# Performance work log

Measured on AMD Instinct MI355X. Metric: run time of the kernel, lower is better.

The kernel has to match this reference:

```python
import jax, jax.numpy as jnp
import numpy as np

N_NODES = 50000
N_EDGES = 800000
IN_NODE = 256
IN_EDGE = 64
OUT_DIM = 128


def setup_inputs() -> dict:
    key = jax.random.key(0)
    k1, k2, k3, k4, k5, k6, k7 = jax.random.split(key, 7)
    feats_node = jax.random.normal(k1, (N_NODES, IN_NODE), dtype=jnp.float32)
    feats_edge = jax.random.normal(k2, (N_EDGES, IN_EDGE), dtype=jnp.float32)
    src = jax.random.randint(k3, (N_EDGES,), 0, N_NODES, dtype=jnp.int32)
    dst = jax.random.randint(k4, (N_EDGES,), 0, N_NODES, dtype=jnp.int32)
    # weights init: normal(std=0.5), torch Linear stores [out, in]
    Wn = 0.5 * jax.random.normal(k5, (OUT_DIM, IN_NODE), dtype=jnp.float32)
    We = 0.5 * jax.random.normal(k6, (IN_EDGE, IN_EDGE), dtype=jnp.float32)
    Wa = 0.5 * jax.random.normal(k7, (1, 2 * OUT_DIM + IN_EDGE), dtype=jnp.float32)
    return {"feats_node": feats_node, "feats_edge": feats_edge,
            "src": src, "dst": dst, "Wn": Wn, "We": We, "Wa": Wa}


def reference(feats_node, feats_edge, src, dst, Wn, We, Wa):
    n_nodes = feats_node.shape[0]
    # node / edge projections
    z = feats_node @ Wn.T            # [N, out_dim]
    ze = feats_edge @ We.T           # [E, in_dim_edge]
    # per-edge attention logit: attn_fc(cat(z_src, z_dst, z_edge)) + leaky_relu
    z3 = jnp.concatenate([z[src], z[dst], ze], axis=1)   # [E, 2*out+edge]
    a = z3 @ Wa.T                                        # [E, 1]
    e = jax.nn.leaky_relu(a, negative_slope=0.2)[:, 0]   # [E]
    # segment softmax over incoming edges of each dst node (numerically stable)
    m = jax.ops.segment_max(e, dst, num_segments=n_nodes)        # [N]
    m = jnp.where(jnp.isfinite(m), m, 0.0)                       # isolated nodes
    e_exp = jnp.exp(e - m[dst])                                  # [E]
    denom = jax.ops.segment_sum(e_exp, dst, num_segments=n_nodes)  # [N]
    alpha = e_exp / jnp.maximum(denom[dst], 1e-38)               # [E]
    # weighted scatter-sum of source messages
    h = jax.ops.segment_sum(alpha[:, None] * z[src], dst, num_segments=n_nodes)
    return h, ze
```

## Files before the change

### kernel.cpp

```cpp
#include <hip/hip_runtime.h>
#include <hip/hip_bf16.h>
#include <math.h>

#define N_NODES 50000
#define N_EDGES 800000
#define IN_NODE 256
#define IN_EDGE 64
#define OUT_DIM 128

#define K1_MT 64
#define K1_KT 32

__global__ __launch_bounds__(256) void k1_node_gemm(
    const float* __restrict__ fn, const float* __restrict__ Wn,
    const float* __restrict__ Wa,
    __hip_bfloat16* __restrict__ zb,
    float* __restrict__ s_src, float* __restrict__ s_dst)
{
    __shared__ float A_s[K1_KT][K1_MT + 4];
    __shared__ float B_s[K1_KT][OUT_DIM + 4];
    __shared__ float red_s[K1_MT][17];
    __shared__ float red_d[K1_MT][17];

    const int t  = threadIdx.x;
    const int m0 = blockIdx.x * K1_MT;
    const int tn = t & 15;
    const int tm = t >> 4;
    const int r0 = tm * 4;
    const int c0 = tn * 8;

    float acc[4][8];
    for (int i = 0; i < 4; ++i)
        for (int j = 0; j < 8; ++j) acc[i][j] = 0.f;

    for (int k0 = 0; k0 < IN_NODE; k0 += K1_KT) {
        {
            const int chunk = t & 7;
            const int nd    = t >> 3;
            for (int hh = 0; hh < 2; ++hh) {
                const int node = nd + hh * 32;
                int gr = m0 + node; if (gr >= N_NODES) gr = N_NODES - 1;
                const float4 v = *(const float4*)&fn[(size_t)gr * IN_NODE + k0 + chunk * 4];
                A_s[chunk * 4 + 0][node] = v.x;
                A_s[chunk * 4 + 1][node] = v.y;
                A_s[chunk * 4 + 2][node] = v.z;
                A_s[chunk * 4 + 3][node] = v.w;
            }
        }
        {
            const int chunk = t & 7;
            const int cb    = t >> 3;
            for (int hh = 0; hh < 4; ++hh) {
                const int c = cb + hh * 32;
                const float4 v = *(const float4*)&Wn[(size_t)c * IN_NODE + k0 + chunk * 4];
                B_s[chunk * 4 + 0][c] = v.x;
                B_s[chunk * 4 + 1][c] = v.y;
                B_s[chunk * 4 + 2][c] = v.z;
                B_s[chunk * 4 + 3][c] = v.w;
            }
        }
        __syncthreads();

        for (int k = 0; k < K1_KT; ++k) {
            const float4 a  = *(const float4*)&A_s[k][r0];
            const float4 b0 = *(const float4*)&B_s[k][c0];
            const float4 b1 = *(const float4*)&B_s[k][c0 + 4];
            const float av[4] = {a.x, a.y, a.z, a.w};
            const float bv[8] = {b0.x, b0.y, b0.z, b0.w, b1.x, b1.y, b1.z, b1.w};
            for (int i = 0; i < 4; ++i)
                for (int j = 0; j < 8; ++j)
                    acc[i][j] += av[i] * bv[j];
        }
        __syncthreads();
    }

    float wa_s[8], wa_d[8];
    for (int j = 0; j < 8; ++j) {
        wa_s[j] = Wa[c0 + j];
        wa_d[j] = Wa[OUT_DIM + c0 + j];
    }
    float ps[4], pd[4];
    for (int i = 0; i < 4; ++i) {
        float a = 0.f, b = 0.f;
        for (int j = 0; j < 8; ++j) {
            a += wa_s[j] * acc[i][j];
            b += wa_d[j] * acc[i][j];
        }
        ps[i] = a; pd[i] = b;
    }

    for (int i = 0; i < 4; ++i) {
        const int node = m0 + r0 + i;
        if (node < N_NODES) {
            alignas(16) __hip_bfloat16 tmp[8];
            for (int j = 0; j < 8; ++j) tmp[j] = __float2bfloat16(acc[i][j]);
            *(uint4*)&zb[(size_t)node * OUT_DIM + c0] = *(const uint4*)tmp;
        }
    }

    for (int i = 0; i < 4; ++i) {
        red_s[r0 + i][tn] = ps[i];
        red_d[r0 + i][tn] = pd[i];
    }
    __syncthreads();
    if (t < K1_MT) {
        const int node = m0 + t;
        if (node < N_NODES) {
            float a = 0.f, b = 0.f;
            for (int j = 0; j < 16; ++j) { a += red_s[t][j]; b += red_d[t][j]; }
            s_src[node] = a;
            s_dst[node] = b;
        }
    }
}

__global__ __launch_bounds__(256) void k2_edge_gemm(
    const float* __restrict__ fe, const float* __restrict__ We,
    const float* __restrict__ Wa,
    float* __restrict__ ze_out, float* __restrict__ s_e)
{
    __shared__ float A_s[IN_EDGE][64 + 4];
    __shared__ float B_s[IN_EDGE][64 + 4];
    __shared__ float red[64][17];

    const int t  = threadIdx.x;
    const size_t e0 = (size_t)blockIdx.x * 64;

    {
        const int chunk = t & 15;
        const int eb    = t >> 4;
        for (int hh = 0; hh < 4; ++hh) {
            const int ed = eb + hh * 16;
            const float4 v = *(const float4*)&fe[(e0 + ed) * IN_EDGE + chunk * 4];
            A_s[chunk * 4 + 0][ed] = v.x;
            A_s[chunk * 4 + 1][ed] = v.y;
            A_s[chunk * 4 + 2][ed] = v.z;
            A_s[chunk * 4 + 3][ed] = v.w;
        }
    }
    {
        const int chunk = t & 15;
        const int cb    = t >> 4;
        for (int hh = 0; hh < 4; ++hh) {
            const int c = cb + hh * 16;
            const float4 v = *(const float4*)&We[(size_t)c * IN_EDGE + chunk * 4];
            B_s[chunk * 4 + 0][c] = v.x;
            B_s[chunk * 4 + 1][c] = v.y;
            B_s[chunk * 4 + 2][c] = v.z;
            B_s[chunk * 4 + 3][c] = v.w;
        }
    }
    __syncthreads();

    const int tn = t & 15, tm = t >> 4;
    const int r0 = tm * 4, c0 = tn * 4;
    float acc[4][4];
    for (int i = 0; i < 4; ++i)
        for (int j = 0; j < 4; ++j) acc[i][j] = 0.f;

    for (int k = 0; k < IN_EDGE; ++k) {
        const float4 a = *(const float4*)&A_s[k][r0];
        const float4 b = *(const float4*)&B_s[k][c0];
        const float av[4] = {a.x, a.y, a.z, a.w};
        const float bv[4] = {b.x, b.y, b.z, b.w};
        for (int i = 0; i < 4; ++i)
            for (int j = 0; j < 4; ++j)
                acc[i][j] += av[i] * bv[j];
    }

    for (int i = 0; i < 4; ++i) {
        float4 v = make_float4(acc[i][0], acc[i][1], acc[i][2], acc[i][3]);
        *(float4*)&ze_out[(e0 + r0 + i) * IN_EDGE + c0] = v;
    }

    float wa[4];
    for (int j = 0; j < 4; ++j) wa[j] = Wa[2 * OUT_DIM + c0 + j];
    for (int i = 0; i < 4; ++i) {
        float pv = 0.f;
        for (int j = 0; j < 4; ++j) pv += wa[j] * acc[i][j];
        red[r0 + i][tn] = pv;
    }
    __syncthreads();
    if (t < 64) {
        float sum = 0.f;
        for (int j = 0; j < 16; ++j) sum += red[t][j];
        s_e[e0 + t] = sum;
    }
}

__global__ void k3_degree(const int* __restrict__ dst, int* __restrict__ deg)
{
    const int i = blockIdx.x * blockDim.x + threadIdx.x;
    if (i < N_EDGES) atomicAdd(&deg[dst[i]], 1);
}

#define SCAN_T 1024
#define SCAN_C 49

__global__ __launch_bounds__(SCAN_T) void k4_scan(
    const int* __restrict__ deg, int* __restrict__ off, int* __restrict__ cursor)
{
    __shared__ int part[SCAN_T];
    const int t = threadIdx.x;
    const int lo = t * SCAN_C;
    int hi = lo + SCAN_C; if (hi > N_NODES) hi = N_NODES;

    int s = 0;
    for (int i = lo; i < hi; ++i) s += deg[i];
    part[t] = s;
    __syncthreads();
    for (int d = 1; d < SCAN_T; d <<= 1) {
        int v = 0;
        if (t >= d) v = part[t - d];
        __syncthreads();
        if (t >= d) part[t] += v;
        __syncthreads();
    }
    int run = (t == 0) ? 0 : part[t - 1];
    for (int i = lo; i < hi; ++i) {
        off[i] = run; cursor[i] = run;
        run += deg[i];
    }
    if (t == SCAN_T - 1) off[N_NODES] = part[SCAN_T - 1];
}

__global__ void k5_fill(
    const int* __restrict__ src, const int* __restrict__ dst,
    const float* __restrict__ s_src, const float* __restrict__ s_dst,
    const float* __restrict__ s_e, int* __restrict__ cursor,
    int* __restrict__ csr_src, float* __restrict__ csr_e)
{
    const int i = blockIdx.x * blockDim.x + threadIdx.x;
    if (i >= N_EDGES) return;
    const int d = dst[i];
    const int s = src[i];
    const int pos = atomicAdd(&cursor[d], 1);
    csr_src[pos] = s;
    float e = s_src[s] + s_dst[d] + s_e[i];
    e = (e > 0.f) ? e : 0.2f * e;
    csr_e[pos] = e;
}

__global__ __launch_bounds__(256) void k6_aggregate(
    const int* __restrict__ off, const int* __restrict__ csr_src,
    const float* __restrict__ csr_e, const __hip_bfloat16* __restrict__ zb,
    float* __restrict__ h)
{
    const int wave = (int)((blockIdx.x * blockDim.x + threadIdx.x) >> 6);
    const int lane = threadIdx.x & 63;
    if (wave >= N_NODES) return;

    const int beg = off[wave];
    const int end = off[wave + 1];
    const int deg = end - beg;

    float2 acc = make_float2(0.f, 0.f);
    if (deg > 0) {
        float m = -INFINITY;
        for (int j = lane; j < deg; j += 64) m = fmaxf(m, csr_e[beg + j]);
        for (int o = 32; o > 0; o >>= 1) m = fmaxf(m, __shfl_xor(m, o, 64));

        float l = 0.f;
        for (int j = 0; j < deg; ++j) {
            const int s = csr_src[beg + j];
            const float w = __expf(csr_e[beg + j] - m);
            l += w;
            const __hip_bfloat162 zp =
                *(const __hip_bfloat162*)&zb[(size_t)s * OUT_DIM + lane * 2];
            const float2 zv = __bfloat1622float2(zp);
            acc.x += w * zv.x;
            acc.y += w * zv.y;
        }
        const float inv = 1.f / fmaxf(l, 1e-38f);
        acc.x *= inv; acc.y *= inv;
    }
    *(float2*)&h[(size_t)wave * OUT_DIM + lane * 2] = acc;
}

extern "C" void kernel_launch(void* const* d_in, const int* in_sizes, int n_in,
                              void* d_out, int out_size, void* d_ws, size_t ws_size,
                              hipStream_t stream)
{
    const float* fn  = (const float*)d_in[0];
    const float* fe  = (const float*)d_in[1];
    const int*   src = (const int*)d_in[2];
    const int*   dst = (const int*)d_in[3];
    const float* Wn  = (const float*)d_in[4];
    const float* We  = (const float*)d_in[5];
    const float* Wa  = (const float*)d_in[6];

    float* h_out  = (float*)d_out;
    float* ze_out = h_out + (size_t)N_NODES * OUT_DIM;

    char* p = (char*)d_ws;
    auto alloc = [&](size_t bytes) -> char* {
        char* r = p;
        p += (bytes + 255) & ~(size_t)255;
        return r;
    };
    __hip_bfloat16* zb   = (__hip_bfloat16*)alloc((size_t)N_NODES * OUT_DIM * 2);
    float* s_src   = (float*)alloc((size_t)N_NODES * 4);
    float* s_dst   = (float*)alloc((size_t)N_NODES * 4);
    float* s_e     = (float*)alloc((size_t)N_EDGES * 4);
    int*   deg     = (int*)alloc((size_t)N_NODES * 4);
    int*   off     = (int*)alloc((size_t)(N_NODES + 1) * 4);
    int*   cursor  = (int*)alloc((size_t)N_NODES * 4);
    int*   csr_src = (int*)alloc((size_t)N_EDGES * 4);
    float* csr_e   = (float*)alloc((size_t)N_EDGES * 4);

    hipMemsetAsync(deg, 0, (size_t)N_NODES * sizeof(int), stream);

    k1_node_gemm<<<(N_NODES + K1_MT - 1) / K1_MT, 256, 0, stream>>>(
        fn, Wn, Wa, zb, s_src, s_dst);
    k2_edge_gemm<<<N_EDGES / 64, 256, 0, stream>>>(fe, We, Wa, ze_out, s_e);
    k3_degree<<<(N_EDGES + 255) / 256, 256, 0, stream>>>(dst, deg);
    k4_scan<<<1, SCAN_T, 0, stream>>>(deg, off, cursor);
    k5_fill<<<(N_EDGES + 255) / 256, 256, 0, stream>>>(
        src, dst, s_src, s_dst, s_e, cursor, csr_src, csr_e);
    k6_aggregate<<<(N_NODES + 3) / 4, 256, 0, stream>>>(
        off, csr_src, csr_e, zb, h_out);
}
```

Measured before the change: 741.5 us.

## Use bf16 MFMA for edge GEMM, fold attention vector, fuse degree count

```diff
diff --git a/kernel.cpp b/kernel.cpp
--- a/kernel.cpp
+++ b/kernel.cpp
@@ -7,6 +7,34 @@
 #define IN_NODE 256
 #define IN_EDGE 64
 #define OUT_DIM 128
+
+typedef __attribute__((ext_vector_type(8))) short short8;
+typedef __attribute__((ext_vector_type(4))) float f32x4;
+
+__device__ inline short f2bf(float x) {
+    union { float f; unsigned u; } v; v.f = x;
+    unsigned r = v.u + 0x7fff + ((v.u >> 16) & 1);
+    return (short)(r >> 16);
+}
+
+__device__ inline void cvt_store8(short* p, float4 a, float4 b) {
+    union { short h[8]; uint4 u; } t;
+    t.h[0] = f2bf(a.x); t.h[1] = f2bf(a.y); t.h[2] = f2bf(a.z); t.h[3] = f2bf(a.w);
+    t.h[4] = f2bf(b.x); t.h[5] = f2bf(b.y); t.h[6] = f2bf(b.z); t.h[7] = f2bf(b.w);
+    *(uint4*)p = t.u;
+}
+
+__global__ void k0_ve(const float* __restrict__ We, const float* __restrict__ Wa,
+                      float* __restrict__ v_e)
+{
+    const int k = threadIdx.x;
+    if (k < IN_EDGE) {
+        float s = 0.f;
+        for (int c = 0; c < IN_EDGE; ++c)
+            s += We[c * IN_EDGE + k] * Wa[2 * OUT_DIM + c];
+        v_e[k] = s;
+    }
+}
 
 #define K1_MT 64
 #define K1_KT 32
@@ -114,84 +142,79 @@
     }
 }
 
-__global__ __launch_bounds__(256) void k2_edge_gemm(
+__global__ __launch_bounds__(256) void k2_edge_gemm_mfma(
     const float* __restrict__ fe, const float* __restrict__ We,
-    const float* __restrict__ Wa,
+    const float* __restrict__ v_e,
+    const int* __restrict__ dst, int* __restrict__ deg,
     float* __restrict__ ze_out, float* __restrict__ s_e)
 {
-    __shared__ float A_s[IN_EDGE][64 + 4];
-    __shared__ float B_s[IN_EDGE][64 + 4];
-    __shared__ float red[64][17];
-
-    const int t  = threadIdx.x;
-    const size_t e0 = (size_t)blockIdx.x * 64;
+    __shared__ alignas(16) short A_lds[128][72];
+    __shared__ alignas(16) short B_lds[64][72];
+
+    const int t    = threadIdx.x;
+    const int lane = t & 63;
+    const int w    = t >> 6;
+    const long e0  = (long)blockIdx.x * 128;
+
+    if (t < 128) atomicAdd(&deg[dst[e0 + t]], 1);
 
     {
-        const int chunk = t & 15;
-        const int eb    = t >> 4;
-        for (int hh = 0; hh < 4; ++hh) {
-            const int ed = eb + hh * 16;
-            const float4 v = *(const float4*)&fe[(e0 + ed) * IN_EDGE + chunk * 4];
-            A_s[chunk * 4 + 0][ed] = v.x;
-            A_s[chunk * 4 + 1][ed] = v.y;
-            A_s[chunk * 4 + 2][ed] = v.z;
-            A_s[chunk * 4 + 3][ed] = v.w;
-        }
+        const int edge = t >> 1, half = t & 1;
+        const float4* rp = (const float4*)&fe[(e0 + edge) * IN_EDGE + half * 32];
+        float4 va[8];
+        for (int q = 0; q < 8; ++q) va[q] = rp[q];
+
+        float part = 0.f;
+        for (int q = 0; q < 8; ++q) {
+            const float4 w4 = *(const float4*)&v_e[half * 32 + q * 4];
+            part += va[q].x * w4.x + va[q].y * w4.y
+                  + va[q].z * w4.z + va[q].w * w4.w;
+        }
+        const float other = __shfl_xor(part, 1, 64);
+        if (half == 0) s_e[e0 + edge] = part + other;
+
+        short* wp = &A_lds[edge][half * 32];
+        for (int q = 0; q < 4; ++q)
+            cvt_store8(wp + q * 8, va[2 * q], va[2 * q + 1]);
     }
     {
-        const int chunk = t & 15;
-        const int cb    = t >> 4;
-        for (int hh = 0; hh < 4; ++hh) {
-            const int c = cb + hh * 16;
-            const float4 v = *(const float4*)&We[(size_t)c * IN_EDGE + chunk * 4];
-            B_s[chunk * 4 + 0][c] = v.x;
-            B_s[chunk * 4 + 1][c] = v.y;
-            B_s[chunk * 4 + 2][c] = v.z;
-            B_s[chunk * 4 + 3][c] = v.w;
-        }
+        const int row = t >> 2, kq = (t & 3) * 16;
+        const float4* rp = (const float4*)&We[(size_t)row * IN_EDGE + kq];
+        cvt_store8(&B_lds[row][kq + 0], rp[0], rp[1]);
+        cvt_store8(&B_lds[row][kq + 8], rp[2], rp[3]);
     }
     __syncthreads();
 
-    const int tn = t & 15, tm = t >> 4;
-    const int r0 = tm * 4, c0 = tn * 4;
-    float acc[4][4];
-    for (int i = 0; i < 4; ++i)
-        for (int j = 0; j < 4; ++j) acc[i][j] = 0.f;
-
-    for (int k = 0; k < IN_EDGE; ++k) {
-        const float4 a = *(const float4*)&A_s[k][r0];
-        const float4 b = *(const float4*)&B_s[k][c0];
-        const float av[4] = {a.x, a.y, a.z, a.w};
-        const float bv[4] = {b.x, b.y, b.z, b.w};
-        for (int i = 0; i < 4; ++i)
-            for (int j = 0; j < 4; ++j)
-                acc[i][j] += av[i] * bv[j];
-    }
-
-    for (int i = 0; i < 4; ++i) {
-        float4 v = make_float4(acc[i][0], acc[i][1], acc[i][2], acc[i][3]);
-        *(float4*)&ze_out[(e0 + r0 + i) * IN_EDGE + c0] = v;
-    }
-
-    float wa[4];
-    for (int j = 0; j < 4; ++j) wa[j] = Wa[2 * OUT_DIM + c0 + j];
-    for (int i = 0; i < 4; ++i) {
-        float pv = 0.f;
-        for (int j = 0; j < 4; ++j) pv += wa[j] * acc[i][j];
-        red[r0 + i][tn] = pv;
-    }
-    __syncthreads();
-    if (t < 64) {
-        float sum = 0.f;
-        for (int j = 0; j < 16; ++j) sum += red[t][j];
-        s_e[e0 + t] = sum;
-    }
-}
-
-__global__ void k3_degree(const int* __restrict__ dst, int* __restrict__ deg)
-{
-    const int i = blockIdx.x * blockDim.x + threadIdx.x;
-    if (i < N_EDGES) atomicAdd(&deg[dst[i]], 1);
+    const int lrow = lane & 15;
+    const int lk   = (lane >> 4) * 8;
+
+    f32x4 acc[2][4];
+    for (int r = 0; r < 2; ++r)
+        for (int c = 0; c < 4; ++c)
+            acc[r][c] = (f32x4){0.f, 0.f, 0.f, 0.f};
+
+    for (int s = 0; s < 2; ++s) {
+        const int kk = s * 32 + lk;
+        short8 aF[2], bF[4];
+        for (int r = 0; r < 2; ++r)
+            aF[r] = *(const short8*)&A_lds[w * 32 + r * 16 + lrow][kk];
+        for (int c = 0; c < 4; ++c)
+            bF[c] = *(const short8*)&B_lds[c * 16 + lrow][kk];
+        for (int r = 0; r < 2; ++r)
+            for (int c = 0; c < 4; ++c)
+                acc[r][c] = __builtin_amdgcn_mfma_f32_16x16x32_bf16(
+                    aF[r], bF[c], acc[r][c], 0, 0, 0);
+    }
+
+    const int rquad = lane >> 4;
+    for (int r = 0; r < 2; ++r) {
+        for (int c = 0; c < 4; ++c) {
+            for (int reg = 0; reg < 4; ++reg) {
+                const long row = e0 + w * 32 + r * 16 + rquad * 4 + reg;
+                ze_out[row * IN_EDGE + c * 16 + lrow] = acc[r][c][reg];
+            }
+        }
+    }
 }
 
 #define SCAN_T 1024
@@ -298,7 +321,7 @@
         p += (bytes + 255) & ~(size_t)255;
         return r;
     };
-    __hip_bfloat16* zb   = (__hip_bfloat16*)alloc((size_t)N_NODES * OUT_DIM * 2);
+    __hip_bfloat16* zb = (__hip_bfloat16*)alloc((size_t)N_NODES * OUT_DIM * 2);
     float* s_src   = (float*)alloc((size_t)N_NODES * 4);
     float* s_dst   = (float*)alloc((size_t)N_NODES * 4);
     float* s_e     = (float*)alloc((size_t)N_EDGES * 4);
@@ -307,13 +330,15 @@
     int*   cursor  = (int*)alloc((size_t)N_NODES * 4);
     int*   csr_src = (int*)alloc((size_t)N_EDGES * 4);
     float* csr_e   = (float*)alloc((size_t)N_EDGES * 4);
+    float* v_e     = (float*)alloc((size_t)IN_EDGE * 4);
 
     hipMemsetAsync(deg, 0, (size_t)N_NODES * sizeof(int), stream);
 
+    k0_ve<<<1, 64, 0, stream>>>(We, Wa, v_e);
     k1_node_gemm<<<(N_NODES + K1_MT - 1) / K1_MT, 256, 0, stream>>>(
         fn, Wn, Wa, zb, s_src, s_dst);
-    k2_edge_gemm<<<N_EDGES / 64, 256, 0, stream>>>(fe, We, Wa, ze_out, s_e);
-    k3_degree<<<(N_EDGES + 255) / 256, 256, 0, stream>>>(dst, deg);
+    k2_edge_gemm_mfma<<<N_EDGES / 128, 256, 0, stream>>>(
+        fe, We, v_e, dst, deg, ze_out, s_e);
     k4_scan<<<1, SCAN_T, 0, stream>>>(deg, off, cursor);
     k5_fill<<<(N_EDGES + 255) / 256, 256, 0, stream>>>(
         src, dst, s_src, s_dst, s_e, cursor, csr_src, csr_e);
```

After: 711.1 us. 1.04x faster.
